# Optimization experiments

Measured on AMD Instinct MI355X. Metric: run time of the kernel, lower is better.

The kernel has to match this reference:

```python
import jax, jax.numpy as jnp
import numpy as np

K = 9      # kernel size
DIL = 2    # dilation
PAD = 8    # padding -> same-size output


def unfold(x):
    """nd2col: (B,C,H,W) -> (B,C,K,K,H,W) patches with dilation/padding."""
    B, C, H, W = x.shape
    xp = jnp.pad(x, ((0, 0), (0, 0), (PAD, PAD), (PAD, PAD)))
    cols = jnp.stack(
        [xp[:, :, i * DIL:i * DIL + H, j * DIL:j * DIL + W]
         for i in range(K) for j in range(K)], axis=2)
    return cols.reshape(B, C, K, K, H, W)


def pac_kernel(f):
    """Gaussian adaptive kernel: exp(-0.5*||f_nbr - f_center||^2), shape (B,1,K,K,H,W)."""
    # center of the dilated patch (K//2, K//2) is the pixel itself
    d = unfold(f) - f[:, :, None, None, :, :]
    return jnp.exp(-0.5 * jnp.sum(d * d, axis=1, keepdims=True))


def pacconv(x, k, w, b):
    """Pixel-adaptive conv: unfold, modulate by guidance kernel, contract with weight."""
    cols = unfold(x)                                  # (B,Cin,K,K,H,W)
    out = jnp.einsum('bcklhw,ockl->bohw', cols * k, w)
    return out + b[None, :, None, None]


def setup_inputs() -> dict:
    key = jax.random.key(0)
    ks = jax.random.split(key, 6)
    B, C, H, W = 1, 32, 128, 128
    x = jax.random.normal(ks[0], (B, C, H, W), jnp.float32)
    f = jax.random.normal(ks[1], (B, C, H, W), jnp.float32)
    fan_in = C * K * K
    bound = float(1.0 / np.sqrt(fan_in))
    W1 = jax.random.uniform(ks[2], (32, C, K, K), jnp.float32, -bound, bound)
    b1 = jax.random.uniform(ks[3], (32,), jnp.float32, -bound, bound)
    W2 = jax.random.uniform(ks[4], (32, 32, K, K), jnp.float32, -bound, bound)
    b2 = jax.random.uniform(ks[5], (32,), jnp.float32, -bound, bound)
    return {"x": x, "f": f, "W1": W1, "b1": b1, "W2": W2, "b2": b2}


def reference(x, f, W1, b1, W2, b2):
    k = pac_kernel(f)  # same guidance for both layers -> identical kernel
    h = pacconv(x, k, W1, b1)
    return pacconv(h, k, W2, b2)
```

## Files before the change

kernel.cpp:

```cpp
#include <hip/hip_runtime.h>

#define HH 128
#define WW 128
#define NPIX 16384
#define NC 32
#define NO 32
#define KS 9
#define TAPS 81
#define DIL 2
#define PAD 8
#define SMAX 27.6310211159f
#define NW (NO * NC * TAPS)
#define CAP 262144

#define BUILD_MASK32(P, M0, M1) do {                                        \
        const uint4* mp_ = (const uint4*)(mask32 + (size_t)(P) * 32);       \
        uint4 ma_ = mp_[0], mb_ = mp_[1];                                   \
        unsigned w_[8] = { ma_.x, ma_.y, ma_.z, ma_.w,                      \
                           mb_.x, mb_.y, mb_.z, mb_.w };                    \
        M0 = 0ull; M1 = 0u;                                                 \
        unsigned m9_[9];                                                    \
        _Pragma("unroll")                                                   \
        for (int i_ = 0; i_ < 9; ++i_) {                                    \
            int k0_ = 3 * i_, k1_ = 3 * i_ + 1, k2_ = 3 * i_ + 2;           \
            unsigned b0_ = (w_[k0_ >> 2] >> ((k0_ & 3) * 8)) & 7u;          \
            unsigned b1_ = (w_[k1_ >> 2] >> ((k1_ & 3) * 8)) & 7u;          \
            unsigned b2_ = (w_[k2_ >> 2] >> ((k2_ & 3) * 8)) & 7u;          \
            m9_[i_] = b0_ | (b1_ << 3) | (b2_ << 6);                        \
        }                                                                   \
        _Pragma("unroll")                                                   \
        for (int i_ = 0; i_ < 7; ++i_)                                      \
            M0 |= (unsigned long long)m9_[i_] << (9 * i_);                  \
        M0 |= (unsigned long long)(m9_[7] & 1u) << 63;                      \
        M1 = (m9_[7] >> 1) | (m9_[8] << 8);                                 \
    } while (0)

__global__ __launch_bounds__(256) void prep3_kernel(
    const float* __restrict__ x, const float* __restrict__ f,
    const float* __restrict__ W1, const float* __restrict__ W2,
    float* __restrict__ xT, float* __restrict__ kbuf,
    unsigned char* __restrict__ mask32,
    float* __restrict__ W1t, float* __restrict__ W2t)
{
    const int bid = blockIdx.x;
    const int tid = threadIdx.x;

    if (bid < 1728) {
        const int pixblk = bid & 63, iz = bid >> 6;
        const int i = iz / 3, z = iz - 3 * i;
        const int pix = pixblk * 256 + tid;
        const int hh = pix >> 7, ww = pix & (WW - 1);
        float fc[NC];
#pragma unroll
        for (int c = 0; c < NC; ++c) fc[c] = f[c * NPIX + pix];
        const int qh = hh + i * DIL - PAD;
        const bool vh = (unsigned)qh < HH;
        unsigned pmask = 0;
#pragma unroll
        for (int jj = 0; jj < 3; ++jj) {
            int j = 3 * z + jj;
            int qw = ww + j * DIL - PAD;
            bool valid = vh & ((unsigned)qw < WW);
            int q = valid ? (qh * WW + qw) : pix;
            float s0 = 0.f, s1 = 0.f, s2 = 0.f, s3 = 0.f;
#pragma unroll
            for (int c4 = 0; c4 < 8; ++c4) {
                float d0 = f[(4 * c4 + 0) * NPIX + q] - fc[4 * c4 + 0];
                float d1 = f[(4 * c4 + 1) * NPIX + q] - fc[4 * c4 + 1];
                float d2 = f[(4 * c4 + 2) * NPIX + q] - fc[4 * c4 + 2];
                float d3 = f[(4 * c4 + 3) * NPIX + q] - fc[4 * c4 + 3];
                s0 = fmaf(d0, d0, s0); s1 = fmaf(d1, d1, s1);
                s2 = fmaf(d2, d2, s2); s3 = fmaf(d3, d3, s3);
            }
            float s = (s0 + s1) + (s2 + s3);
            bool live = valid && (s <= SMAX) && !(i == 4 && j == 4);
            if (live) {
                pmask |= 1u << jj;
                kbuf[(i * KS + j) * NPIX + pix] = __expf(-0.5f * s);
            }
        }
        mask32[(size_t)pix * 32 + iz] = (unsigned char)pmask;
        return;
    }

    if (bid < 1792) {
        for (int t = (bid - 1728) * 256 + tid; t < NW; t += 64 * 256) {
            int o = t / (NC * TAPS);
            int r = t - o * (NC * TAPS);
            int c = r / TAPS;
            int tap = r - c * TAPS;
            int d = (tap * NO + o) * NC + c;
            W1t[d] = W1[t];
            W2t[d] = W2[t];
        }
        return;
    }

    for (int idx = (bid - 1792) * 256 + tid; idx < NPIX * NC; idx += 64 * 256) {
        int p = idx >> 5, c = idx & 31;
        xT[idx] = x[c * NPIX + p];
    }
}

__global__ __launch_bounds__(256) void layer_kernel(
    const float* __restrict__ inT, const float* __restrict__ kbuf,
    const unsigned char* __restrict__ mask32, const float* __restrict__ Wt,
    const float* __restrict__ bias, float* __restrict__ outp, int strided)
{
    const int hw = threadIdx.x >> 5;
    const int lane = threadIdx.x & 31;
    const int p = blockIdx.x * 8 + hw;

    unsigned long long A0; unsigned A1;
    BUILD_MASK32(p, A0, A1);

    float acc = bias[lane];

#define TAP_BODY(T, Q, KV) do {                                            \
        const float4* xp_ = (const float4*)(inT + (Q) * NC);               \
        const float4* wp_ = (const float4*)(Wt + ((T) * NO + lane) * NC);  \
        float t0_ = 0.f, t1_ = 0.f, t2_ = 0.f, t3_ = 0.f;                  \
        _Pragma("unroll")                                                  \
        for (int c4_ = 0; c4_ < 8; ++c4_) {                                \
            float4 x4_ = xp_[c4_];                                         \
            float4 w4_ = wp_[c4_];                                         \
            t0_ = fmaf(w4_.x, x4_.x, t0_);                                 \
            t1_ = fmaf(w4_.y, x4_.y, t1_);                                 \
            t2_ = fmaf(w4_.z, x4_.z, t2_);                                 \
            t3_ = fmaf(w4_.w, x4_.w, t3_);                                 \
        }                                                                  \
        acc = fmaf((KV), (t0_ + t1_) + (t2_ + t3_), acc);                  \
    } while (0)

    TAP_BODY(40, p, 1.0f);

    while (A0) {
        int T = __builtin_ctzll(A0);
        A0 &= A0 - 1;
        int ii = T / KS, jj = T - KS * ii;
        int q = p + (ii * DIL - PAD) * WW + (jj * DIL - PAD);
        float kv = kbuf[T * NPIX + p];
        TAP_BODY(T, q, kv);
    }
    while (A1) {
        int T = 64 + __builtin_ctz(A1);
        A1 &= A1 - 1;
        int ii = T / KS, jj = T - KS * ii;
        int q = p + (ii * DIL - PAD) * WW + (jj * DIL - PAD);
        float kv = kbuf[T * NPIX + p];
        TAP_BODY(T, q, kv);
    }
#undef TAP_BODY

    if (strided) outp[lane * NPIX + p] = acc;
    else         outp[p * NC + lane] = acc;
}

__global__ __launch_bounds__(64) void zero_cnt_kernel(unsigned* __restrict__ cnt)
{
    if (threadIdx.x == 0) *cnt = 0u;
}

__device__ __forceinline__ void sparse_body(
    const float* __restrict__ in, const float* __restrict__ Wt,
    const unsigned* __restrict__ cnt, const uint2* __restrict__ list,
    float* __restrict__ out, unsigned gid, unsigned stride)
{
    unsigned n = *cnt;
    if (n > CAP) n = CAP;
    const unsigned total = n * 32u;
    for (unsigned it = gid; it < total; it += stride) {
        unsigned e = it >> 5;
        int o = (int)(it & 31u);
        uint2 me = list[e];
        int pix = (int)(me.x & 16383u);
        int T = (int)(me.x >> 14);
        float kv = __uint_as_float(me.y);
        int ii = T / KS, jj = T - KS * ii;
        int q = pix + (ii * DIL - PAD) * WW + (jj * DIL - PAD);
        const float4* __restrict__ wp =
            (const float4*)(Wt + (T * NO + o) * NC);
        float t0 = 0.f, t1 = 0.f, t2 = 0.f, t3 = 0.f;
#pragma unroll
        for (int c4 = 0; c4 < 8; ++c4) {
            float4 w4 = wp[c4];
            t0 = fmaf(in[(4 * c4 + 0) * NPIX + q], w4.x, t0);
            t1 = fmaf(in[(4 * c4 + 1) * NPIX + q], w4.y, t1);
            t2 = fmaf(in[(4 * c4 + 2) * NPIX + q], w4.z, t2);
            t3 = fmaf(in[(4 * c4 + 3) * NPIX + q], w4.w, t3);
        }
        atomicAdd(&out[o * NPIX + pix], kv * ((t0 + t1) + (t2 + t3)));
    }
}

__global__ __launch_bounds__(256) void front_kernel(
    const float* __restrict__ x, const float* __restrict__ f,
    const float* __restrict__ W1, const float* __restrict__ W2,
    const float* __restrict__ b1,
    float* __restrict__ h, unsigned* __restrict__ cnt,
    uint2* __restrict__ list, float* __restrict__ W1t,
    float* __restrict__ W2t, float* __restrict__ outz)
{
    const int y = blockIdx.y;
    const int tid = threadIdx.x;

    if (y < 41) {
        const int pix = blockIdx.x * 256 + tid;
        const int hh = pix >> 7, ww = pix & (WW - 1);
        float fc[NC];
#pragma unroll
        for (int c = 0; c < NC; ++c) fc[c] = f[c * NPIX + pix];
#pragma unroll
        for (int u = 0; u < 2; ++u) {
            int T = 2 * y + u;
            if (T >= TAPS || T == 40) continue;
            int ii = T / KS, jj = T - KS * ii;
            int qh = hh + ii * DIL - PAD;
            int qw = ww + jj * DIL - PAD;
            bool valid = ((unsigned)qh < HH) & ((unsigned)qw < WW);
            int q = valid ? (qh * WW + qw) : pix;
            float s0 = 0.f, s1 = 0.f, s2 = 0.f, s3 = 0.f;
#pragma unroll
            for (int c4 = 0; c4 < 8; ++c4) {
                float d0 = f[(4 * c4 + 0) * NPIX + q] - fc[4 * c4 + 0];
                float d1 = f[(4 * c4 + 1) * NPIX + q] - fc[4 * c4 + 1];
                float d2 = f[(4 * c4 + 2) * NPIX + q] - fc[4 * c4 + 2];
                float d3 = f[(4 * c4 + 3) * NPIX + q] - fc[4 * c4 + 3];
                s0 = fmaf(d0, d0, s0); s1 = fmaf(d1, d1, s1);
                s2 = fmaf(d2, d2, s2); s3 = fmaf(d3, d3, s3);
            }
            float s = (s0 + s1) + (s2 + s3);
            if (valid && (s <= SMAX)) {
                unsigned idx = atomicAdd(cnt, 1u);
                if (idx < CAP)
                    list[idx] = make_uint2(
                        (unsigned)pix | ((unsigned)T << 14),
                        __float_as_uint(__expf(-0.5f * s)));
            }
        }
        return;
    }

    if (y < 49) {
        const int o0 = (y - 41) * 4;
        __shared__ float wsm[4 * NC];
        if (tid < 128) {
            int o = tid >> 5, c = tid & 31;
            wsm[tid] = W1[((o0 + o) * NC + c) * TAPS + 40];
        }
        __syncthreads();
        const int pix = blockIdx.x * 256 + tid;
        float x0[NC];
#pragma unroll
        for (int c = 0; c < NC; ++c) x0[c] = x[c * NPIX + pix];
        float a0 = 0.f, a1 = 0.f, a2 = 0.f, a3 = 0.f;
#pragma unroll
        for (int c = 0; c < NC; ++c) {
            float xv = x0[c];
            a0 = fmaf(xv, wsm[0 * NC + c], a0);
            a1 = fmaf(xv, wsm[1 * NC + c], a1);
            a2 = fmaf(xv, wsm[2 * NC + c], a2);
            a3 = fmaf(xv, wsm[3 * NC + c], a3);
        }
        h[(o0 + 0) * NPIX + pix] = a0 + b1[o0 + 0];
        h[(o0 + 1) * NPIX + pix] = a1 + b1[o0 + 1];
        h[(o0 + 2) * NPIX + pix] = a2 + b1[o0 + 2];
        h[(o0 + 3) * NPIX + pix] = a3 + b1[o0 + 3];
        return;
    }

    if (y == 49) {
        float4 z = make_float4(0.f, 0.f, 0.f, 0.f);
        for (int t = blockIdx.x * 256 + tid; t < (NO * NPIX) / 4; t += 64 * 256)
            ((float4*)outz)[t] = z;
        return;
    }

    for (int t = blockIdx.x * 256 + tid; t < NW; t += 64 * 256) {
        int o = t / (NC * TAPS);
        int r = t - o * (NC * TAPS);
        int c = r / TAPS;
        int tap = r - c * TAPS;
        int d = (tap * NO + o) * NC + c;
        W1t[d] = W1[t];
        W2t[d] = W2[t];
    }
}

__global__ __launch_bounds__(256) void sparse1_kernel(
    const float* __restrict__ x, const float* __restrict__ W1t,
    const unsigned* __restrict__ cnt, const uint2* __restrict__ list,
    float* __restrict__ h)
{
    sparse_body(x, W1t, cnt, list, h,
                blockIdx.x * 256 + threadIdx.x, gridDim.x * 256);
}

__global__ __launch_bounds__(256) void back_kernel(
    const float* __restrict__ h, const float* __restrict__ W2,
    const float* __restrict__ W2t, const float* __restrict__ b2,
    const unsigned* __restrict__ cnt, const uint2* __restrict__ list,
    float* __restrict__ out)
{
    const int y = blockIdx.y;
    const int tid = threadIdx.x;
    if (y < 8) {
        const int o0 = y * 4;
        __shared__ float wsm[4 * NC];
        if (tid < 128) {
            int o = tid >> 5, c = tid & 31;
            wsm[tid] = W2[((o0 + o) * NC + c) * TAPS + 40];
        }
        __syncthreads();
        const int pix = blockIdx.x * 256 + tid;
        float h0[NC];
#pragma unroll
        for (int c = 0; c < NC; ++c) h0[c] = h[c * NPIX + pix];
        float a0 = 0.f, a1 = 0.f, a2 = 0.f, a3 = 0.f;
#pragma unroll
        for (int c = 0; c < NC; ++c) {
            float hv = h0[c];
            a0 = fmaf(hv, wsm[0 * NC + c], a0);
            a1 = fmaf(hv, wsm[1 * NC + c], a1);
            a2 = fmaf(hv, wsm[2 * NC + c], a2);
            a3 = fmaf(hv, wsm[3 * NC + c], a3);
        }
        atomicAdd(&out[(o0 + 0) * NPIX + pix], a0 + b2[o0 + 0]);
        atomicAdd(&out[(o0 + 1) * NPIX + pix], a1 + b2[o0 + 1]);
        atomicAdd(&out[(o0 + 2) * NPIX + pix], a2 + b2[o0 + 2]);
        atomicAdd(&out[(o0 + 3) * NPIX + pix], a3 + b2[o0 + 3]);
        return;
    }
    sparse_body(h, W2t, cnt, list, out,
                blockIdx.x * 256 + tid, 64 * 256);
}

#define CHUNK 27
#define NCHUNK 3
#define KMIN 1e-6f
__global__ __launch_bounds__(256) void pac_layer_fuse(
    const float* __restrict__ in, const float* __restrict__ f,
    const float* __restrict__ Wt, const float* __restrict__ bias,
    float* __restrict__ out)
{
    __shared__ float wl[NC * CHUNK * 8];
    const int og = blockIdx.y;
    const int pix = blockIdx.x * 256 + threadIdx.x;
    const int h = pix >> 7, w = pix & (WW - 1);
    float acc[8];
#pragma unroll
    for (int i = 0; i < 8; ++i) acc[i] = 0.f;
    float fc[NC];
#pragma unroll
    for (int c = 0; c < NC; ++c) fc[c] = f[c * NPIX + pix];
    for (int ch = 0; ch < NCHUNK; ++ch) {
        __syncthreads();
        for (int idx = threadIdx.x; idx < NC * CHUNK * 8; idx += 256) {
            int t = idx % CHUNK;
            int c = (idx / CHUNK) % NC;
            int o = idx / (CHUNK * NC);
            wl[(c * CHUNK + t) * 8 + o] =
                Wt[(og * 8 + o) * (NC * TAPS) + c * TAPS + ch * CHUNK + t];
        }
        __syncthreads();
        for (int t = 0; t < CHUNK; ++t) {
            int tap = ch * CHUNK + t;
            int qh = h + (tap / KS) * DIL - PAD;
            int qw = w + (tap % KS) * DIL - PAD;
            bool valid = ((unsigned)qh < HH) & ((unsigned)qw < WW);
            int q = qh * WW + qw;
            float s = 0.f;
#pragma unroll
            for (int c = 0; c < NC; ++c) {
                float fn = valid ? f[c * NPIX + q] : 0.f;
                float d = fn - fc[c];
                s = fmaf(d, d, s);
            }
            float kv = __expf(-0.5f * s);
            if (__all((kv < KMIN) | (!valid))) continue;
            const float* wpp = &wl[t * 8];
#pragma unroll 8
            for (int c = 0; c < NC; ++c) {
                float v = valid ? in[c * NPIX + q] : 0.f;
                v *= kv;
#pragma unroll
                for (int o = 0; o < 8; ++o)
                    acc[o] = fmaf(v, wpp[c * CHUNK * 8 + o], acc[o]);
            }
        }
    }
#pragma unroll
    for (int o = 0; o < 8; ++o)
        out[(og * 8 + o) * NPIX + pix] = acc[o] + bias[og * 8 + o];
}

extern "C" void kernel_launch(void* const* d_in, const int* in_sizes, int n_in,
                              void* d_out, int out_size, void* d_ws, size_t ws_size,
                              hipStream_t stream)
{
    (void)in_sizes; (void)n_in; (void)out_size;
    const float* x  = (const float*)d_in[0];
    const float* f  = (const float*)d_in[1];
    const float* W1 = (const float*)d_in[2];
    const float* b1 = (const float*)d_in[3];
    const float* W2 = (const float*)d_in[4];
    const float* b2 = (const float*)d_in[5];
    float* out = (float*)d_out;

    float* ws = (float*)d_ws;
    float* xT   = ws;
    float* hT   = xT + NPIX * NC;
    float* kbuf = hT + NPIX * NO;
    float* W1t  = kbuf + TAPS * NPIX;
    float* W2t  = W1t + NW;
    unsigned char* mask32 = (unsigned char*)(W2t + NW);
    const size_t need_main =
        (size_t)(NPIX * NC + NPIX * NO + TAPS * NPIX + 2 * NW) * 4
        + (size_t)NPIX * 32;
    float* hA   = ws;
    float* W1tA = ws + NO * NPIX;
    float* W2tA = W1tA + NW;
    unsigned* cnt = (unsigned*)(W2tA + NW);
    uint2* list = (uint2*)(cnt + 16);
    const size_t need_fb =
        (size_t)(NO * NPIX + 2 * NW + 16) * 4 + (size_t)CAP * 8;

    if (ws_size >= need_main) {
        prep3_kernel<<<dim3(1856), 256, 0, stream>>>(
            x, f, W1, W2, xT, kbuf, mask32, W1t, W2t);
        layer_kernel<<<dim3(2048), 256, 0, stream>>>(
            xT, kbuf, mask32, W1t, b1, hT, 0);
        layer_kernel<<<dim3(2048), 256, 0, stream>>>(
            hT, kbuf, mask32, W2t, b2, out, 1);
    } else if (ws_size >= need_fb) {
        zero_cnt_kernel<<<dim3(1), 64, 0, stream>>>(cnt);
        front_kernel<<<dim3(64, 51), 256, 0, stream>>>(
            x, f, W1, W2, b1, hA, cnt, list, W1tA, W2tA, out);
        sparse1_kernel<<<dim3(128), 256, 0, stream>>>(x, W1tA, cnt, list, hA);
        back_kernel<<<dim3(64, 9), 256, 0, stream>>>(
            hA, W2, W2tA, b2, cnt, list, out);
    } else {
        float* hbuf = ws;
        pac_layer_fuse<<<dim3(64, 4), 256, 0, stream>>>(x, f, W1, b1, hbuf);
        pac_layer_fuse<<<dim3(64, 4), 256, 0, stream>>>(hbuf, f, W2, b2, out);
    }
}
```

Measured before the change: 118.9 us.

## Fuse both PAC conv layers into one kernel, recomputing hidden activations per tap

```diff
diff --git a/kernel.cpp b/kernel.cpp
--- a/kernel.cpp
+++ b/kernel.cpp
@@ -102,58 +102,93 @@
     }
 }
 
-__global__ __launch_bounds__(256) void layer_kernel(
-    const float* __restrict__ inT, const float* __restrict__ kbuf,
-    const unsigned char* __restrict__ mask32, const float* __restrict__ Wt,
-    const float* __restrict__ bias, float* __restrict__ outp, int strided)
-{
-    const int hw = threadIdx.x >> 5;
-    const int lane = threadIdx.x & 31;
-    const int p = blockIdx.x * 8 + hw;
+__global__ __launch_bounds__(256) void fused2_kernel(
+    const float* __restrict__ xT, const float* __restrict__ kbuf,
+    const unsigned char* __restrict__ mask32,
+    const float* __restrict__ W1t, const float* __restrict__ W2t,
+    const float* __restrict__ b1, const float* __restrict__ b2,
+    float* __restrict__ out)
+{
+    const int wv = threadIdx.x >> 6;
+    const int lane = threadIdx.x & 63;
+    const int half = lane >> 5;
+    const int o = lane & 31;
+    const int c0 = half * 16;
+    const int p = blockIdx.x * 4 + wv;
+    __shared__ float hlds[4][NC];
+
+    const float b1o = b1[o];
+
+#define DOT16(WROW, XROW, RES) do {                                        \
+        const float4* wq_ = (const float4*)((WROW) + c0);                  \
+        const float4* xq_ = (const float4*)((XROW) + c0);                  \
+        float r0_ = 0.f, r1_ = 0.f, r2_ = 0.f, r3_ = 0.f;                  \
+        _Pragma("unroll")                                                  \
+        for (int k_ = 0; k_ < 4; ++k_) {                                   \
+            float4 w4_ = wq_[k_], x4_ = xq_[k_];                           \
+            r0_ = fmaf(w4_.x, x4_.x, r0_);                                 \
+            r1_ = fmaf(w4_.y, x4_.y, r1_);                                 \
+            r2_ = fmaf(w4_.z, x4_.z, r2_);                                 \
+            r3_ = fmaf(w4_.w, x4_.w, r3_);                                 \
+        }                                                                  \
+        RES = (r0_ + r1_) + (r2_ + r3_);                                   \
+    } while (0)
 
     unsigned long long A0; unsigned A1;
     BUILD_MASK32(p, A0, A1);
-
-    float acc = bias[lane];
-
-#define TAP_BODY(T, Q, KV) do {                                            \
-        const float4* xp_ = (const float4*)(inT + (Q) * NC);               \
-        const float4* wp_ = (const float4*)(Wt + ((T) * NO + lane) * NC);  \
-        float t0_ = 0.f, t1_ = 0.f, t2_ = 0.f, t3_ = 0.f;                  \
-        _Pragma("unroll")                                                  \
-        for (int c4_ = 0; c4_ < 8; ++c4_) {                                \
-            float4 x4_ = xp_[c4_];                                         \
-            float4 w4_ = wp_[c4_];                                         \
-            t0_ = fmaf(w4_.x, x4_.x, t0_);                                 \
-            t1_ = fmaf(w4_.y, x4_.y, t1_);                                 \
-            t2_ = fmaf(w4_.z, x4_.z, t2_);                                 \
-            t3_ = fmaf(w4_.w, x4_.w, t3_);                                 \
-        }                                                                  \
-        acc = fmaf((KV), (t0_ + t1_) + (t2_ + t3_), acc);                  \
-    } while (0)
-
-    TAP_BODY(40, p, 1.0f);
-
-    while (A0) {
-        int T = __builtin_ctzll(A0);
-        A0 &= A0 - 1;
-        int ii = T / KS, jj = T - KS * ii;
-        int q = p + (ii * DIL - PAD) * WW + (jj * DIL - PAD);
-        float kv = kbuf[T * NPIX + p];
-        TAP_BODY(T, q, kv);
-    }
-    while (A1) {
-        int T = 64 + __builtin_ctz(A1);
-        A1 &= A1 - 1;
-        int ii = T / KS, jj = T - KS * ii;
-        int q = p + (ii * DIL - PAD) * WW + (jj * DIL - PAD);
-        float kv = kbuf[T * NPIX + p];
-        TAP_BODY(T, q, kv);
-    }
-#undef TAP_BODY
-
-    if (strided) outp[lane * NPIX + p] = acc;
-    else         outp[p * NC + lane] = acc;
+    unsigned long long A0s = A0; unsigned A1s = A1;
+
+    float acc = 0.f;
+    int first = 1;
+    for (;;) {
+        int Tq, q; float kvq;
+        if (first)      { Tq = 40; q = p; kvq = 1.0f; }
+        else if (A0s) {
+            Tq = __builtin_ctzll(A0s); A0s &= A0s - 1;
+            int ii = Tq / KS, jj = Tq - KS * ii;
+            q = p + (ii * DIL - PAD) * WW + (jj * DIL - PAD);
+            kvq = kbuf[Tq * NPIX + p];
+        } else if (A1s) {
+            Tq = 64 + __builtin_ctz(A1s); A1s &= A1s - 1;
+            int ii = Tq / KS, jj = Tq - KS * ii;
+            q = p + (ii * DIL - PAD) * WW + (jj * DIL - PAD);
+            kvq = kbuf[Tq * NPIX + p];
+        } else break;
+
+        unsigned long long B0; unsigned B1;
+        if (first) { B0 = A0; B1 = A1; }
+        else BUILD_MASK32(q, B0, B1);
+
+        float hpart;
+        DOT16(W1t + (40 * NO + o) * NC, xT + q * NC, hpart);
+        while (B0) {
+            int T2 = __builtin_ctzll(B0); B0 &= B0 - 1;
+            int i2 = T2 / KS, j2 = T2 - KS * i2;
+            int q2 = q + (i2 * DIL - PAD) * WW + (j2 * DIL - PAD);
+            float kv2 = kbuf[T2 * NPIX + q];
+            float d; DOT16(W1t + (T2 * NO + o) * NC, xT + q2 * NC, d);
+            hpart = fmaf(kv2, d, hpart);
+        }
+        while (B1) {
+            int T2 = 64 + __builtin_ctz(B1); B1 &= B1 - 1;
+            int i2 = T2 / KS, j2 = T2 - KS * i2;
+            int q2 = q + (i2 * DIL - PAD) * WW + (j2 * DIL - PAD);
+            float kv2 = kbuf[T2 * NPIX + q];
+            float d; DOT16(W1t + (T2 * NO + o) * NC, xT + q2 * NC, d);
+            hpart = fmaf(kv2, d, hpart);
+        }
+        float hfull = hpart + __shfl_xor(hpart, 32);
+        hfull += b1o;
+        if (half == 0) hlds[wv][o] = hfull;
+        float wsdot;
+        DOT16(W2t + (Tq * NO + o) * NC, &hlds[wv][0], wsdot);
+        acc = fmaf(kvq, wsdot, acc);
+        first = 0;
+    }
+#undef DOT16
+
+    float accf = acc + __shfl_xor(acc, 32);
+    if (half == 0) out[o * NPIX + p] = accf + b2[o];
 }
 
 __global__ __launch_bounds__(64) void zero_cnt_kernel(unsigned* __restrict__ cnt)
@@ -409,13 +444,12 @@
 
     float* ws = (float*)d_ws;
     float* xT   = ws;
-    float* hT   = xT + NPIX * NC;
-    float* kbuf = hT + NPIX * NO;
+    float* kbuf = xT + NPIX * NC;
     float* W1t  = kbuf + TAPS * NPIX;
     float* W2t  = W1t + NW;
     unsigned char* mask32 = (unsigned char*)(W2t + NW);
     const size_t need_main =
-        (size_t)(NPIX * NC + NPIX * NO + TAPS * NPIX + 2 * NW) * 4
+        (size_t)(NPIX * NC + TAPS * NPIX + 2 * NW) * 4
         + (size_t)NPIX * 32;
     float* hA   = ws;
     float* W1tA = ws + NO * NPIX;
@@ -428,10 +462,8 @@
     if (ws_size >= need_main) {
         prep3_kernel<<<dim3(1856), 256, 0, stream>>>(
             x, f, W1, W2, xT, kbuf, mask32, W1t, W2t);
-        layer_kernel<<<dim3(2048), 256, 0, stream>>>(
-            xT, kbuf, mask32, W1t, b1, hT, 0);
-        layer_kernel<<<dim3(2048), 256, 0, stream>>>(
-            hT, kbuf, mask32, W2t, b2, out, 1);
+        fused2_kernel<<<dim3(NPIX / 4), 256, 0, stream>>>(
+            xT, kbuf, mask32, W1t, W2t, b1, b2, out);
     } else if (ws_size >= need_fb) {
         zero_cnt_kernel<<<dim3(1), 64, 0, stream>>>(cnt);
         front_kernel<<<dim3(64, 51), 256, 0, stream>>>(
```

New measurement: 120.1 us. Within noise of the previous version (+1.0%).
